# Optimization experiments

Measured on AMD Instinct MI355X. Metric: run time of the kernel, lower is better.

The kernel has to match this reference:

```python
import jax, jax.numpy as jnp
import numpy as np

N_HEADS = 8  # from init_kwargs; only used for the softmax scale


def setup_inputs() -> dict:
    key = jax.random.key(0)
    k1, k2, k3 = jax.random.split(key, 3)
    B, S, D = 4, 4096, 1024
    inputs = jax.random.normal(k1, (B, S, 2 * D), dtype=jnp.float32)
    W_qkv = jax.random.normal(k2, (2 * D, 3 * D), dtype=jnp.float32) * (1.0 / np.sqrt(2 * D))
    W_ff = jax.random.normal(k3, (D, D), dtype=jnp.float32) * (1.0 / np.sqrt(D))
    b_ff = jnp.zeros((D,), dtype=jnp.float32)
    return {"inputs": inputs, "W_qkv": W_qkv, "W_ff": W_ff, "b_ff": b_ff}


def reference(inputs, W_qkv, W_ff, b_ff):
    D = W_ff.shape[0]
    dim_head = D / N_HEADS
    scale = 1.0 / np.sqrt(dim_head)
    kqv = inputs @ W_qkv                       # [B, S, 3D]
    k, q, v = jnp.split(kqv, 3, axis=-1)        # chunk order in source: k, q, v
    scores = jnp.einsum('bqd,bkd->bqk', q, k) * scale   # [B, S, S]
    attn = jax.nn.softmax(scores, axis=-1)
    # dropout_p is undefined in the buggy source; treated as eval-mode identity
    out = jnp.einsum('bqk,bkd->bqd', attn, v)   # [B, S, D]
    return out @ W_ff + b_ff
```

## Files before the change

### kernel.cpp

```cpp
#include <hip/hip_runtime.h>

typedef unsigned short u16;
using bf16x8 = __attribute__((ext_vector_type(8))) __bf16;
using f32x4  = __attribute__((ext_vector_type(4))) float;
using u16x8  = __attribute__((ext_vector_type(8))) u16;

__device__ __forceinline__ u16 f2bf(float f) {
    unsigned u = __builtin_bit_cast(unsigned, f);
    u += 0x7FFFu + ((u >> 16) & 1u);
    return (u16)(u >> 16);
}
__device__ __forceinline__ float bf2f(u16 h) {
    unsigned u = ((unsigned)h) << 16;
    return __builtin_bit_cast(float, u);
}
__device__ __forceinline__ u16 to_bf(float f) { return f2bf(f); }
__device__ __forceinline__ u16 to_bf(u16 h)   { return h; }

__device__ __forceinline__ void gload_lds16(const u16* g, u16* l) {
    __builtin_amdgcn_global_load_lds(
        (const __attribute__((address_space(1))) unsigned int*)g,
        (__attribute__((address_space(3))) unsigned int*)l,
        16, 0, 0);
}

__global__ __launch_bounds__(256) void k_cvt_f32_bf16(const float* __restrict__ in,
                                                      u16* __restrict__ out, long n) {
    long i = ((long)blockIdx.x * 256 + threadIdx.x) * 8;
    if (i + 8 > n) return;
    f32x4 a = *(const f32x4*)(in + i);
    f32x4 b = *(const f32x4*)(in + i + 4);
    u16x8 o;
    o[0] = f2bf(a[0]); o[1] = f2bf(a[1]); o[2] = f2bf(a[2]); o[3] = f2bf(a[3]);
    o[4] = f2bf(b[0]); o[5] = f2bf(b[1]); o[6] = f2bf(b[2]); o[7] = f2bf(b[3]);
    *(u16x8*)(out + i) = o;
}

template <typename T>
__global__ __launch_bounds__(256) void k_transpose_bf16(
    const T* __restrict__ in, long in_rs, long in_bs,
    u16* __restrict__ out, long out_rs, long out_bs, int R, int C) {
    __shared__ u16 tile[32][33];
    const int b = blockIdx.z;
    const T* ip = in + (long)b * in_bs;
    u16* op = out + (long)b * out_bs;
    const int tx = threadIdx.x, ty = threadIdx.y;
    const long r0 = (long)blockIdx.y * 32, c0 = (long)blockIdx.x * 32;
#pragma unroll
    for (int i = 0; i < 4; ++i) {
        int r = ty + i * 8;
        tile[r][tx] = to_bf(ip[(r0 + r) * in_rs + c0 + tx]);
    }
    __syncthreads();
#pragma unroll
    for (int i = 0; i < 4; ++i) {
        int c = ty + i * 8;
        op[(c0 + c) * out_rs + r0 + tx] = tile[tx][c];
    }
}

__global__ __launch_bounds__(256) void k_psum_recip(const float* __restrict__ psum,
                                                    float* __restrict__ rrow,
                                                    int nx, long total) {
    long idx = (long)blockIdx.x * 256 + threadIdx.x;
    if (idx >= total) return;
    const long z = idx >> 12, row = idx & 4095;
    const float* p = psum + (z * nx) * 4096 + row;
    float s = 0.f;
    for (int x = 0; x < nx; ++x) s += p[(long)x * 4096];
    rrow[idx] = 1.0f / s;
}


#define VMC(n) asm volatile("s_waitcnt vmcnt(" #n ")" ::: "memory")
#define SCHB   __builtin_amdgcn_sched_barrier(0)
#define BAR    __builtin_amdgcn_s_barrier()
#define PRIO1  __builtin_amdgcn_s_setprio(1)
#define PRIO0  __builtin_amdgcn_s_setprio(0)
#define SWZ(b) ((b) ^ ((((b) >> 9) & 1) << 5))

template <int EPI>
__global__ __launch_bounds__(512, 4) void k_gemm3b(
    const u16* __restrict__ Ag, long lda, long sA,
    const u16* __restrict__ Bg, long ldb, long sB,
    void* __restrict__ Cv, long ldc, long sC,
    int K, float scale, const float* __restrict__ rrowZ, long sR,
    const float* __restrict__ bias, float* __restrict__ psum) {
    __shared__ __align__(16) u16 As[3][128 * 32];
    __shared__ __align__(16) u16 Bs[3][256 * 32];

    const int tid = threadIdx.x;
    const int lane = tid & 63, wid = tid >> 6;
    const int wm = wid >> 2, wn = wid & 3;
    const int z = blockIdx.z;
    const long m0 = (long)blockIdx.y * 128;
    const long n0 = (long)blockIdx.x * 256;
    const u16* A = Ag + (long)z * sA;
    const u16* B = Bg + (long)z * sB;

    long aSrc, bSrc0, bSrc1;
    {
        int dg = SWZ(tid * 16);
        aSrc = (m0 + (dg >> 6)) * lda + ((dg & 63) >> 1);
        bSrc0 = (n0 + (dg >> 6)) * ldb + ((dg & 63) >> 1);
        dg = SWZ(8192 + tid * 16);
        bSrc1 = (n0 + (dg >> 6)) * ldb + ((dg & 63) >> 1);
    }
    const int r16 = lane & 15, g = lane >> 4;
    const int vA = SWZ((wm * 64 + r16) * 64 + g * 16);
    const int vB = SWZ((wn * 64 + r16) * 64 + g * 16);

#define STG(bb, kt) do { \
        gload_lds16(A + aSrc + (kt), &As[bb][wid * 512]); \
        gload_lds16(B + bSrc0 + (kt), &Bs[bb][wid * 512]); \
        gload_lds16(B + bSrc1 + (kt), &Bs[bb][4096 + wid * 512]); } while (0)
#define LD4_A(bb) do { _Pragma("unroll") for (int _i = 0; _i < 4; ++_i) \
        afr[_i] = *(const bf16x8*)((const char*)&As[bb][0] + vA + _i * 1024); } while (0)
#define LD4_B(bb) do { _Pragma("unroll") for (int _i = 0; _i < 4; ++_i) \
        bfr[_i] = *(const bf16x8*)((const char*)&Bs[bb][0] + vB + _i * 1024); } while (0)
#define MM16() do { \
        _Pragma("unroll") for (int mf = 0; mf < 4; ++mf) \
        _Pragma("unroll") for (int nf = 0; nf < 4; ++nf) \
            acc[mf][nf] = __builtin_amdgcn_mfma_f32_16x16x32_bf16( \
                afr[mf], bfr[nf], acc[mf][nf], 0, 0, 0); } while (0)

    f32x4 acc[4][4] = {};
    bf16x8 afr[4], bfr[4];

    const int NT = K >> 5;
    STG(0, 0); STG(1, 32);
    VMC(3); SCHB;
    BAR; SCHB;

    int b0 = 0, b1 = 1, b2 = 2;
    for (int t = 0; t < NT; ++t) {
        LD4_A(b0); LD4_B(b0);
        if (t + 2 < NT) STG(b2, (long)(t + 2) * 32);
        PRIO1; MM16(); PRIO0;
        if (t + 2 < NT) { VMC(3); }
        else if (t + 1 < NT) { VMC(0); }
        BAR; SCHB;
        int tm = b0; b0 = b1; b1 = b2; b2 = tm;
    }

    const int r_in = (lane >> 4) * 4;
    const int c_in = lane & 15;
    const float* rr = (EPI == 2) ? (rrowZ + (long)z * sR) : nullptr;
    float rsum[4][4];
    if constexpr (EPI == 1) {
#pragma unroll
        for (int a = 0; a < 4; ++a)
#pragma unroll
            for (int b = 0; b < 4; ++b) rsum[a][b] = 0.f;
    }
#pragma unroll
    for (int mf = 0; mf < 4; ++mf) {
#pragma unroll
        for (int nf = 0; nf < 4; ++nf) {
            const long cg = n0 + wn * 64 + nf * 16 + c_in;
#pragma unroll
            for (int j = 0; j < 4; ++j) {
                const long rg = m0 + wm * 64 + mf * 16 + r_in + j;
                float v = acc[mf][nf][j];
                if constexpr (EPI == 0) {
                    ((u16*)Cv)[(long)z * sC + rg * ldc + cg] = f2bf(v);
                } else if constexpr (EPI == 1) {
                    float e = __expf(v * scale);
                    ((u16*)Cv)[(long)z * sC + rg * ldc + cg] = f2bf(e);
                    rsum[mf][j] += e;
                } else if constexpr (EPI == 2) {
                    ((u16*)Cv)[(long)z * sC + rg * ldc + cg] = f2bf(v * rr[rg]);
                } else {
                    ((float*)Cv)[(long)z * sC + rg * ldc + cg] = v + bias[cg];
                }
            }
        }
    }
    if constexpr (EPI == 1) {
        float* ps = (float*)&As[0][0];
#pragma unroll
        for (int mf = 0; mf < 4; ++mf) {
#pragma unroll
            for (int j = 0; j < 4; ++j) {
                float s = rsum[mf][j];
#pragma unroll
                for (int w = 1; w < 16; w <<= 1) s += __shfl_xor(s, w);
                if ((lane & 15) == 0)
                    ps[(wm * 64 + mf * 16 + (lane >> 4) * 4 + j) * 4 + wn] = s;
            }
        }
        __syncthreads();
        if (tid < 128) {
            float s = ps[tid * 4] + ps[tid * 4 + 1] + ps[tid * 4 + 2] + ps[tid * 4 + 3];
            const long M = (long)gridDim.y * 128;
            psum[((long)z * gridDim.x + blockIdx.x) * M + m0 + tid] = s;
        }
    }
#undef MM16
#undef LD4_A
#undef LD4_B
#undef STG
}

extern "C" void kernel_launch(void* const* d_in, const int* in_sizes, int n_in,
                              void* d_out, int out_size, void* d_ws, size_t ws_size,
                              hipStream_t stream) {
    (void)in_sizes; (void)n_in; (void)out_size;
    const int S = 4096;
    const long BS = 4L * S;
    const float* x_f    = (const float*)d_in[0];
    const float* Wqkv_f = (const float*)d_in[1];
    const float* Wff_f  = (const float*)d_in[2];
    const float* bff    = (const float*)d_in[3];
    float* out = (float*)d_out;

    const size_t need4 = 67108864UL + 12582912UL + 2097152UL + 100663296UL +
                         33554432UL + 4UL * 33554432UL + 33554432UL + 65536UL +
                         4UL * 16 * 4096 * 4;
    const bool batched = ws_size >= need4;
    const int Z = batched ? 4 : 1;

    char* p = (char*)d_ws;
    u16* x_bf  = (u16*)p; p += BS * 2048 * 2;
    u16* WqkvT = (u16*)p; p += 3072L * 2048 * 2;
    u16* WffT  = (u16*)p; p += 1024L * 1024 * 2;
    u16* kqv   = (u16*)p; p += BS * 3072 * 2;
    u16* vT    = (u16*)p; p += 4L * 1024 * 4096 * 2;
    u16* probs = (u16*)p; p += (long)Z * 4096L * 4096 * 2;
    u16* attn  = (u16*)p; p += BS * 1024 * 2;
    float* rrow = (float*)p; p += (long)Z * 4096L * 4;
    float* psum = (float*)p; p += (long)Z * 16 * 4096 * 4;

    k_cvt_f32_bf16<<<dim3((unsigned)(BS * 2048 / 2048)), 256, 0, stream>>>(x_f, x_bf, BS * 2048);
    k_transpose_bf16<float><<<dim3(3072 / 32, 2048 / 32, 1), dim3(32, 8), 0, stream>>>(
        Wqkv_f, 3072, 0, WqkvT, 2048, 0, 2048, 3072);
    k_transpose_bf16<float><<<dim3(1024 / 32, 1024 / 32, 1), dim3(32, 8), 0, stream>>>(
        Wff_f, 1024, 0, WffT, 1024, 0, 1024, 1024);

    k_gemm3b<0><<<dim3(3072 / 256, 16384 / 128, 1), 512, 0, stream>>>(
        x_bf, 2048, 0, WqkvT, 2048, 0, kqv, 3072, 0, 2048, 0.f, nullptr, 0, nullptr, nullptr);

    k_transpose_bf16<u16><<<dim3(1024 / 32, 4096 / 32, 4), dim3(32, 8), 0, stream>>>(
        kqv + 2048, 3072, (long)S * 3072, vT, 4096, 1024L * 4096, 4096, 1024);

    const float scale = 0.08838834764831845f;
    for (int b = 0; b < 4; b += Z) {
        const u16* kbase = kqv + (long)b * S * 3072;
        k_gemm3b<1><<<dim3(4096 / 256, 4096 / 128, Z), 512, 0, stream>>>(
            kbase + 1024, 3072, (long)S * 3072, kbase, 3072, (long)S * 3072,
            probs, 4096, (long)S * S, 1024, scale, nullptr, 0, nullptr, psum);
        k_psum_recip<<<(Z * 4096 + 255) / 256, 256, 0, stream>>>(
            psum, rrow, 16, (long)Z * 4096);
        k_gemm3b<2><<<dim3(1024 / 256, 4096 / 128, Z), 512, 0, stream>>>(
            probs, 4096, (long)S * S, vT + (long)b * 1024 * 4096, 4096, 1024L * 4096,
            attn + (long)b * S * 1024, 1024, (long)S * 1024,
            4096, 0.f, rrow, 4096, nullptr, nullptr);
    }

    k_gemm3b<3><<<dim3(1024 / 256, 16384 / 128, 1), 512, 0, stream>>>(
        attn, 1024, 0, WffT, 1024, 0, out, 1024, 0, 1024, 0.f, nullptr, 0, bff, nullptr);
}
```

Baseline: 618.4 us.

## Switch GEMMs to 256x128 tiles with 4 waves each computing 128x64

Replaces the 8-wave 128x256 block GEMM with a 4-wave 256x128 block in which each wave computes a 128x64 sub-tile (8x4 MFMA fragments). The aim is more MFMA work per LDS fragment load and fewer waves sharing barriers, which should lift arithmetic intensity per wave. In exchange, register pressure doubles (32 accumulators plus 12 fragment vectors), occupancy falls to 2 blocks per CU, and the softmax partial-sum buffer doubles to 32 column-blocks. The swizzle-add macros reapply SWZ, relying on it being its own inverse.

```diff
diff --git a/kernel.cpp b/kernel.cpp
--- a/kernel.cpp
+++ b/kernel.cpp
@@ -80,64 +80,73 @@
 #define SWZ(b) ((b) ^ ((((b) >> 9) & 1) << 5))
 
 template <int EPI>
-__global__ __launch_bounds__(512, 4) void k_gemm3b(
+__global__ __launch_bounds__(256, 2) void k_gemmw(
     const u16* __restrict__ Ag, long lda, long sA,
     const u16* __restrict__ Bg, long ldb, long sB,
     void* __restrict__ Cv, long ldc, long sC,
     int K, float scale, const float* __restrict__ rrowZ, long sR,
     const float* __restrict__ bias, float* __restrict__ psum) {
-    __shared__ __align__(16) u16 As[3][128 * 32];
-    __shared__ __align__(16) u16 Bs[3][256 * 32];
+    __shared__ __align__(16) u16 As[3][256 * 32];
+    __shared__ __align__(16) u16 Bs[3][128 * 32];
 
     const int tid = threadIdx.x;
     const int lane = tid & 63, wid = tid >> 6;
-    const int wm = wid >> 2, wn = wid & 3;
+    const int wm = wid >> 1, wn = wid & 1;
     const int z = blockIdx.z;
-    const long m0 = (long)blockIdx.y * 128;
-    const long n0 = (long)blockIdx.x * 256;
+    const long m0 = (long)blockIdx.y * 256;
+    const long n0 = (long)blockIdx.x * 128;
     const u16* A = Ag + (long)z * sA;
     const u16* B = Bg + (long)z * sB;
 
-    long aSrc, bSrc0, bSrc1;
-    {
-        int dg = SWZ(tid * 16);
-        aSrc = (m0 + (dg >> 6)) * lda + ((dg & 63) >> 1);
-        bSrc0 = (n0 + (dg >> 6)) * ldb + ((dg & 63) >> 1);
-        dg = SWZ(8192 + tid * 16);
-        bSrc1 = (n0 + (dg >> 6)) * ldb + ((dg & 63) >> 1);
+    long aSrc[4], bSrc[2];
+#pragma unroll
+    for (int c = 0; c < 4; ++c) {
+        int dg = SWZ((wid * 4 + c) * 1024 + lane * 16);
+        aSrc[c] = (m0 + (dg >> 6)) * lda + ((dg & 63) >> 1);
+    }
+#pragma unroll
+    for (int c = 0; c < 2; ++c) {
+        int dg = SWZ((wid * 2 + c) * 1024 + lane * 16);
+        bSrc[c] = (n0 + (dg >> 6)) * ldb + ((dg & 63) >> 1);
     }
     const int r16 = lane & 15, g = lane >> 4;
-    const int vA = SWZ((wm * 64 + r16) * 64 + g * 16);
+    const int vA = SWZ((wm * 128 + r16) * 64 + g * 16);
     const int vB = SWZ((wn * 64 + r16) * 64 + g * 16);
 
 #define STG(bb, kt) do { \
-        gload_lds16(A + aSrc + (kt), &As[bb][wid * 512]); \
-        gload_lds16(B + bSrc0 + (kt), &Bs[bb][wid * 512]); \
-        gload_lds16(B + bSrc1 + (kt), &Bs[bb][4096 + wid * 512]); } while (0)
-#define LD4_A(bb) do { _Pragma("unroll") for (int _i = 0; _i < 4; ++_i) \
-        afr[_i] = *(const bf16x8*)((const char*)&As[bb][0] + vA + _i * 1024); } while (0)
-#define LD4_B(bb) do { _Pragma("unroll") for (int _i = 0; _i < 4; ++_i) \
-        bfr[_i] = *(const bf16x8*)((const char*)&Bs[bb][0] + vB + _i * 1024); } while (0)
-#define MM16() do { \
-        _Pragma("unroll") for (int mf = 0; mf < 4; ++mf) \
-        _Pragma("unroll") for (int nf = 0; nf < 4; ++nf) \
-            acc[mf][nf] = __builtin_amdgcn_mfma_f32_16x16x32_bf16( \
-                afr[mf], bfr[nf], acc[mf][nf], 0, 0, 0); } while (0)
-
-    f32x4 acc[4][4] = {};
-    bf16x8 afr[4], bfr[4];
+        _Pragma("unroll") for (int _c = 0; _c < 4; ++_c) \
+            gload_lds16(A + aSrc[_c] + (kt), &As[bb][(wid * 4 + _c) * 512]); \
+        _Pragma("unroll") for (int _c = 0; _c < 2; ++_c) \
+            gload_lds16(B + bSrc[_c] + (kt), &Bs[bb][(wid * 2 + _c) * 512]); } while (0)
+#define LD12(bb) do { \
+        _Pragma("unroll") for (int _i = 0; _i < 8; ++_i) \
+            afr[_i] = *(const bf16x8*)((const char*)&As[bb][0] + \
+                                       SWZ_ADD(vA, _i * 1024)); \
+        _Pragma("unroll") for (int _i = 0; _i < 4; ++_i) \
+            bfr[_i] = *(const bf16x8*)((const char*)&Bs[bb][0] + \
+                                       SWZ_ADD(vB, _i * 1024)); } while (0)
+#define SWZ_ADD(vbase, add) SWZ(UNSWZ(vbase) + (add))
+#define UNSWZ(b) SWZ(b)
+#define MM32() do { \
+        _Pragma("unroll") for (int _m = 0; _m < 8; ++_m) \
+        _Pragma("unroll") for (int _n = 0; _n < 4; ++_n) \
+            acc[_m][_n] = __builtin_amdgcn_mfma_f32_16x16x32_bf16( \
+                afr[_m], bfr[_n], acc[_m][_n], 0, 0, 0); } while (0)
+
+    f32x4 acc[8][4] = {};
+    bf16x8 afr[8], bfr[4];
 
     const int NT = K >> 5;
     STG(0, 0); STG(1, 32);
-    VMC(3); SCHB;
+    VMC(6); SCHB;
     BAR; SCHB;
 
     int b0 = 0, b1 = 1, b2 = 2;
     for (int t = 0; t < NT; ++t) {
-        LD4_A(b0); LD4_B(b0);
+        LD12(b0);
         if (t + 2 < NT) STG(b2, (long)(t + 2) * 32);
-        PRIO1; MM16(); PRIO0;
-        if (t + 2 < NT) { VMC(3); }
+        PRIO1; MM32(); PRIO0;
+        if (t + 2 < NT) { VMC(6); }
         else if (t + 1 < NT) { VMC(0); }
         BAR; SCHB;
         int tm = b0; b0 = b1; b1 = b2; b2 = tm;
@@ -146,21 +155,21 @@
     const int r_in = (lane >> 4) * 4;
     const int c_in = lane & 15;
     const float* rr = (EPI == 2) ? (rrowZ + (long)z * sR) : nullptr;
-    float rsum[4][4];
+    float rsum[8][4];
     if constexpr (EPI == 1) {
 #pragma unroll
-        for (int a = 0; a < 4; ++a)
+        for (int a = 0; a < 8; ++a)
 #pragma unroll
             for (int b = 0; b < 4; ++b) rsum[a][b] = 0.f;
     }
 #pragma unroll
-    for (int mf = 0; mf < 4; ++mf) {
+    for (int mf = 0; mf < 8; ++mf) {
 #pragma unroll
         for (int nf = 0; nf < 4; ++nf) {
             const long cg = n0 + wn * 64 + nf * 16 + c_in;
 #pragma unroll
             for (int j = 0; j < 4; ++j) {
-                const long rg = m0 + wm * 64 + mf * 16 + r_in + j;
+                const long rg = m0 + wm * 128 + mf * 16 + r_in + j;
                 float v = acc[mf][nf][j];
                 if constexpr (EPI == 0) {
                     ((u16*)Cv)[(long)z * sC + rg * ldc + cg] = f2bf(v);
@@ -179,26 +188,27 @@
     if constexpr (EPI == 1) {
         float* ps = (float*)&As[0][0];
 #pragma unroll
-        for (int mf = 0; mf < 4; ++mf) {
+        for (int mf = 0; mf < 8; ++mf) {
 #pragma unroll
             for (int j = 0; j < 4; ++j) {
                 float s = rsum[mf][j];
 #pragma unroll
                 for (int w = 1; w < 16; w <<= 1) s += __shfl_xor(s, w);
                 if ((lane & 15) == 0)
-                    ps[(wm * 64 + mf * 16 + (lane >> 4) * 4 + j) * 4 + wn] = s;
+                    ps[(wm * 128 + mf * 16 + (lane >> 4) * 4 + j) * 2 + wn] = s;
             }
         }
         __syncthreads();
-        if (tid < 128) {
-            float s = ps[tid * 4] + ps[tid * 4 + 1] + ps[tid * 4 + 2] + ps[tid * 4 + 3];
-            const long M = (long)gridDim.y * 128;
+        const long M = (long)gridDim.y * 256;
+        {
+            float s = ps[tid * 2] + ps[tid * 2 + 1];
             psum[((long)z * gridDim.x + blockIdx.x) * M + m0 + tid] = s;
         }
     }
-#undef MM16
-#undef LD4_A
-#undef LD4_B
+#undef MM32
+#undef LD12
+#undef SWZ_ADD
+#undef UNSWZ
 #undef STG
 }
 
@@ -216,7 +226,7 @@
 
     const size_t need4 = 67108864UL + 12582912UL + 2097152UL + 100663296UL +
                          33554432UL + 4UL * 33554432UL + 33554432UL + 65536UL +
-                         4UL * 16 * 4096 * 4;
+                         4UL * 32 * 4096 * 4;
     const bool batched = ws_size >= need4;
     const int Z = batched ? 4 : 1;
 
@@ -229,7 +239,7 @@
     u16* probs = (u16*)p; p += (long)Z * 4096L * 4096 * 2;
     u16* attn  = (u16*)p; p += BS * 1024 * 2;
     float* rrow = (float*)p; p += (long)Z * 4096L * 4;
-    float* psum = (float*)p; p += (long)Z * 16 * 4096 * 4;
+    float* psum = (float*)p; p += (long)Z * 32 * 4096 * 4;
 
     k_cvt_f32_bf16<<<dim3((unsigned)(BS * 2048 / 2048)), 256, 0, stream>>>(x_f, x_bf, BS * 2048);
     k_transpose_bf16<float><<<dim3(3072 / 32, 2048 / 32, 1), dim3(32, 8), 0, stream>>>(
@@ -237,7 +247,7 @@
     k_transpose_bf16<float><<<dim3(1024 / 32, 1024 / 32, 1), dim3(32, 8), 0, stream>>>(
         Wff_f, 1024, 0, WffT, 1024, 0, 1024, 1024);
 
-    k_gemm3b<0><<<dim3(3072 / 256, 16384 / 128, 1), 512, 0, stream>>>(
+    k_gemmw<0><<<dim3(3072 / 128, 16384 / 256, 1), 256, 0, stream>>>(
         x_bf, 2048, 0, WqkvT, 2048, 0, kqv, 3072, 0, 2048, 0.f, nullptr, 0, nullptr, nullptr);
 
     k_transpose_bf16<u16><<<dim3(1024 / 32, 4096 / 32, 4), dim3(32, 8), 0, stream>>>(
@@ -246,17 +256,17 @@
     const float scale = 0.08838834764831845f;
     for (int b = 0; b < 4; b += Z) {
         const u16* kbase = kqv + (long)b * S * 3072;
-        k_gemm3b<1><<<dim3(4096 / 256, 4096 / 128, Z), 512, 0, stream>>>(
+        k_gemmw<1><<<dim3(4096 / 128, 4096 / 256, Z), 256, 0, stream>>>(
             kbase + 1024, 3072, (long)S * 3072, kbase, 3072, (long)S * 3072,
             probs, 4096, (long)S * S, 1024, scale, nullptr, 0, nullptr, psum);
         k_psum_recip<<<(Z * 4096 + 255) / 256, 256, 0, stream>>>(
-            psum, rrow, 16, (long)Z * 4096);
-        k_gemm3b<2><<<dim3(1024 / 256, 4096 / 128, Z), 512, 0, stream>>>(
+            psum, rrow, 32, (long)Z * 4096);
+        k_gemmw<2><<<dim3(1024 / 128, 4096 / 256, Z), 256, 0, stream>>>(
             probs, 4096, (long)S * S, vT + (long)b * 1024 * 4096, 4096, 1024L * 4096,
             attn + (long)b * S * 1024, 1024, (long)S * 1024,
             4096, 0.f, rrow, 4096, nullptr, nullptr);
     }
 
-    k_gemm3b<3><<<dim3(1024 / 256, 16384 / 128, 1), 512, 0, stream>>>(
+    k_gemmw<3><<<dim3(1024 / 128, 16384 / 256, 1), 256, 0, stream>>>(
         attn, 1024, 0, WffT, 1024, 0, out, 1024, 0, 1024, 0.f, nullptr, 0, bff, nullptr);
 }
```

Result: slower. 680.9 us (+10.1%).
